# Kernel optimization log

Hardware: AMD Instinct MI355X
Metric: run time of the kernel (lower is better)

The kernel has to match this reference:

```python
import jax, jax.numpy as jnp
import numpy as np

IMG = 224          # image_size
FMAP = (56, 56)    # feature_map_dims (AdaptiveAvgPool2d((56,56)))
K_REWEIGHT = 3     # self.n_reweight
BLUR_RADIUS = 4    # KNNGaussianBlur(4): kernel 9, sigma 4


def _cdist(a, b):
    # Euclidean pairwise distance, [Na, D] x [Nb, D] -> [Na, Nb]
    a2 = jnp.sum(a * a, axis=1, keepdims=True)            # [Na,1]
    b2 = jnp.sum(b * b, axis=1, keepdims=True).T          # [1,Nb]
    d2 = a2 + b2 - 2.0 * (a @ b.T)
    return jnp.sqrt(jnp.maximum(d2, 0.0))


def _gaussian_blur(x):
    # x: [1,1,H,W]; torchvision GaussianBlur(kernel=9, sigma=4), reflect pad
    r, sigma = BLUR_RADIUS, float(BLUR_RADIUS)
    t = jnp.arange(2 * r + 1, dtype=x.dtype) - r
    g = jnp.exp(-(t * t) / (2.0 * sigma * sigma))
    g = g / jnp.sum(g)
    k2d = jnp.outer(g, g)[None, None]                     # [1,1,9,9]
    xp = jnp.pad(x, ((0, 0), (0, 0), (r, r), (r, r)), mode='reflect')
    return jax.lax.conv_general_dilated(
        xp, k2d, window_strides=(1, 1), padding='VALID',
        dimension_numbers=('NCHW', 'OIHW', 'NCHW'))


def setup_inputs() -> dict:
    key = jax.random.key(0)
    k1, k2 = jax.random.split(key)
    patch = jax.random.normal(k1, (FMAP[0] * FMAP[1], 768), dtype=jnp.float32)
    patch_lib = jax.random.normal(k2, (16384, 768), dtype=jnp.float32)
    mean = jnp.zeros((), dtype=jnp.float32)
    std = jnp.ones((), dtype=jnp.float32)
    return {"patch": patch, "patch_lib": patch_lib, "mean": mean, "std": std}


def reference(patch, patch_lib, mean, std):
    # normalization (method_name != 'Point_MAE' branch)
    p = (patch - mean) / std                               # [N, D]

    dist = _cdist(p, patch_lib)                            # [N, Nlib]
    min_val = jnp.min(dist, axis=1)                        # [N]
    min_idx = jnp.argmin(dist, axis=1)                     # [N]
    s_idx = jnp.argmax(min_val)
    s_star = jnp.max(min_val)

    m_test = p[s_idx]                                      # [D]
    m_star = patch_lib[min_idx[s_idx]]                     # [D]

    # distances of m_star to whole bank, k smallest
    w_dist = jnp.sqrt(jnp.maximum(
        jnp.sum((patch_lib - m_star) ** 2, axis=1), 0.0))  # [Nlib]
    _, nn_idx = jax.lax.top_k(-w_dist, K_REWEIGHT)         # smallest k
    m_star_knn = jnp.linalg.norm(
        m_test[None, :] - patch_lib[nn_idx[1:]], axis=1)   # [k-1]

    D_sqrt = jnp.sqrt(jnp.asarray(patch.shape[1], dtype=p.dtype))
    w = 1.0 - jnp.exp(s_star / D_sqrt) / jnp.sum(jnp.exp(m_star_knn / D_sqrt))
    s = w * s_star

    s_map = min_val.reshape(1, 1, *FMAP)
    s_map = jax.image.resize(s_map, (1, 1, IMG, IMG), method='bilinear')
    s_map = _gaussian_blur(s_map)
    return s, s_map
```

## Files before the change

### kernel.cpp

```cpp
#include <hip/hip_runtime.h>
#include <hip/hip_bf16.h>
#include <stdint.h>

#define N_PATCH 3136
#define N_PATCH_PAD 3200
#define N_LIB   16384
#define DIM     768
#define IMGSZ   224
#define FM      56

#define BK 32
#define KT 24
#define MT 25
#define NTILES 128

typedef __bf16 bf16_t;
typedef __bf16 bf16x8 __attribute__((ext_vector_type(8)));
typedef __bf16 bf16x4_v __attribute__((ext_vector_type(4)));
typedef float  f32x4  __attribute__((ext_vector_type(4)));

#define FLT_MAX_ 3.402823466e+38f

struct Scal {
  unsigned long long approx_max_pack;
  unsigned long long cand_pack[64];
  int cand[64];
  int cand_count;
};

__device__ __forceinline__ float wave_reduce_sum(float v) {
#pragma unroll
  for (int s = 32; s > 0; s >>= 1) v += __shfl_xor(v, s, 64);
  return v;
}

__device__ __forceinline__ unsigned long long shfl_xor_u64(unsigned long long v, int mask) {
  unsigned lo = (unsigned)v, hi = (unsigned)(v >> 32);
  lo = __shfl_xor(lo, mask, 64);
  hi = __shfl_xor(hi, mask, 64);
  return ((unsigned long long)hi << 32) | lo;
}

__device__ __forceinline__ void async16(const bf16_t* g, bf16_t* l) {
  __builtin_amdgcn_global_load_lds(
      (const __attribute__((address_space(1))) unsigned int*)g,
      (__attribute__((address_space(3))) unsigned int*)l, 16, 0, 0);
}

__global__ void prep_patch_kernel(const float* __restrict__ patch,
                                  const float* __restrict__ meanp,
                                  const float* __restrict__ stdp,
                                  bf16_t* __restrict__ pb, float* __restrict__ a2,
                                  Scal* sc) {
  int t = threadIdx.x;
  int row = blockIdx.x * 4 + (t >> 6);
  int lane = t & 63;
  if (blockIdx.x == 0) {
    if (t < 64) sc->cand_pack[t] = ~0ULL;
    if (t == 0) { sc->approx_max_pack = 0ULL; sc->cand_count = 0; }
  }
  float mu = meanp[0], sd = stdp[0];
  float acc = 0.f;
#pragma unroll
  for (int k = 0; k < 3; k++) {
    float4 v = ((const float4*)(patch + (size_t)row * DIM))[lane + 64 * k];
    v.x = (v.x - mu) / sd; v.y = (v.y - mu) / sd;
    v.z = (v.z - mu) / sd; v.w = (v.w - mu) / sd;
    bf16x4_v o = {(__bf16)v.x, (__bf16)v.y, (__bf16)v.z, (__bf16)v.w};
    *(bf16x4_v*)(pb + (size_t)row * DIM + (lane + 64 * k) * 4) = o;
    acc += v.x*v.x + v.y*v.y + v.z*v.z + v.w*v.w;
  }
  acc = wave_reduce_sum(acc);
  if (lane == 0) a2[row] = acc;
}

__global__ void prep_lib_kernel(const float* __restrict__ lib,
                                bf16_t* __restrict__ lb, float* __restrict__ b2) {
  int t = threadIdx.x;
  int row = blockIdx.x * 4 + (t >> 6);
  int lane = t & 63;
  float acc = 0.f;
#pragma unroll
  for (int k = 0; k < 3; k++) {
    float4 v = ((const float4*)(lib + (size_t)row * DIM))[lane + 64 * k];
    bf16x4_v o = {(__bf16)v.x, (__bf16)v.y, (__bf16)v.z, (__bf16)v.w};
    *(bf16x4_v*)(lb + (size_t)row * DIM + (lane + 64 * k) * 4) = o;
    acc += v.x*v.x + v.y*v.y + v.z*v.z + v.w*v.w;
  }
  acc = wave_reduce_sum(acc);
  if (lane == 0) b2[row] = acc;
}

__global__ __launch_bounds__(256, 3)
void gemm_min_kernel(const bf16_t* __restrict__ pb, const bf16_t* __restrict__ lb,
                     const float* __restrict__ a2, const float* __restrict__ b2,
                     float* __restrict__ part) {
  __shared__ __align__(16) bf16_t As[2][128 * BK];
  __shared__ __align__(16) bf16_t Bs[2][128 * BK];
  __shared__ unsigned smin[128];

  const int t = threadIdx.x;
  const int wave = t >> 6;
  const int lane = t & 63;
  const int l15 = lane & 15;
  const int quad = lane >> 4;
  const int wm = (wave >> 1) * 64;
  const int wn = (wave & 1) * 64;

  const int lid = blockIdx.x;
  const int xcd = lid & 7;
  const int slot = lid >> 3;
  const int ntile = xcd + 8 * (slot / MT);
  const int mtile = slot % MT;
  const int m0 = mtile * 128;
  const int n0 = ntile * 128;

  int ra0 = m0 + (t >> 2);       if (ra0 > N_PATCH - 1) ra0 = N_PATCH - 1;
  int ra1 = m0 + 64 + (t >> 2);  if (ra1 > N_PATCH - 1) ra1 = N_PATCH - 1;
  const bf16_t* gA0 = pb + (size_t)ra0 * DIM + (t & 3) * 8;
  const bf16_t* gA1 = pb + (size_t)ra1 * DIM + (t & 3) * 8;
  const bf16_t* gB0 = lb + (size_t)(n0 + (t >> 2)) * DIM + (t & 3) * 8;
  const bf16_t* gB1 = gB0 + (size_t)64 * DIM;

  if (t < 128) smin[t] = 0xffffffffu;

  {
    bf16_t* la = &As[0][0];
    bf16_t* lb_ = &Bs[0][0];
    async16(gA0, la + t * 8);
    async16(gA1, la + 2048 + t * 8);
    async16(gB0, lb_ + t * 8);
    async16(gB1, lb_ + 2048 + t * 8);
  }
  __syncthreads();

  f32x4 acc[4][4];
#pragma unroll
  for (int mi = 0; mi < 4; mi++)
#pragma unroll
    for (int ni = 0; ni < 4; ni++) { f32x4 z = {0.f,0.f,0.f,0.f}; acc[mi][ni] = z; }

  for (int k = 0; k < KT; ++k) {
    const int cur = k & 1;
    if (k + 1 < KT) {
      const int nxt = cur ^ 1;
      const size_t ko = (size_t)(k + 1) * BK;
      bf16_t* la = &As[nxt][0];
      bf16_t* lb_ = &Bs[nxt][0];
      async16(gA0 + ko, la + t * 8);
      async16(gA1 + ko, la + 2048 + t * 8);
      async16(gB0 + ko, lb_ + t * 8);
      async16(gB1 + ko, lb_ + 2048 + t * 8);
    }

    bf16x8 afr[4], bfr[4];
#pragma unroll
    for (int mi = 0; mi < 4; mi++)
      afr[mi] = *(const bf16x8*)(&As[cur][(wm + mi * 16 + l15) * BK + quad * 8]);
#pragma unroll
    for (int ni = 0; ni < 4; ni++)
      bfr[ni] = *(const bf16x8*)(&Bs[cur][(wn + ni * 16 + l15) * BK + quad * 8]);
#pragma unroll
    for (int mi = 0; mi < 4; mi++)
#pragma unroll
      for (int ni = 0; ni < 4; ni++)
        acc[mi][ni] = __builtin_amdgcn_mfma_f32_16x16x32_bf16(afr[mi], bfr[ni],
                                                              acc[mi][ni], 0, 0, 0);
    __syncthreads();
  }

  float b2n[4];
#pragma unroll
  for (int ni = 0; ni < 4; ni++) b2n[ni] = b2[n0 + wn + ni * 16 + l15];

#pragma unroll
  for (int mi = 0; mi < 4; mi++) {
#pragma unroll
    for (int r = 0; r < 4; r++) {
      int rloc = wm + mi * 16 + quad * 4 + r;
      int mrow = m0 + rloc;
      float a2v = a2[mrow < N_PATCH ? mrow : (N_PATCH - 1)];
      float best = a2v + b2n[0] - 2.0f * acc[mi][0][r];
#pragma unroll
      for (int ni = 1; ni < 4; ni++)
        best = fminf(best, a2v + b2n[ni] - 2.0f * acc[mi][ni][r]);
      best = fmaxf(best, 0.0f);
#pragma unroll
      for (int s = 1; s < 16; s <<= 1)
        best = fminf(best, __shfl_xor(best, s, 64));
      if (l15 == 0) atomicMin(&smin[rloc], __float_as_uint(best));
    }
  }
  __syncthreads();
  if (t < 128) part[(size_t)(m0 + t) * NTILES + ntile] = __uint_as_float(smin[t]);
}

__global__ void finalize_kernel(const float* __restrict__ part,
                                float* __restrict__ min_val, Scal* sc) {
  int t = threadIdx.x;
  int row = blockIdx.x * 4 + (t >> 6);
  int lane = t & 63;
  if (row >= N_PATCH) return;
  uint2 pv = *(const uint2*)(part + (size_t)row * NTILES + lane * 2);
  unsigned m = pv.x < pv.y ? pv.x : pv.y;
#pragma unroll
  for (int s = 1; s < 64; s <<= 1) {
    unsigned o = __shfl_xor((int)m, s, 64);
    if (o < m) m = o;
  }
  if (lane == 0) {
    float v = sqrtf(__uint_as_float(m));
    min_val[row] = v;
    unsigned long long mp = (((unsigned long long)__float_as_uint(v)) << 32) |
                            (unsigned)(0xffffffffu - (unsigned)row);
    atomicMax(&sc->approx_max_pack, mp);
  }
}

__global__ void collect_kernel(const float* __restrict__ min_val, Scal* sc) {
  int i = blockIdx.x * 256 + threadIdx.x;
  if (i >= N_PATCH) return;
  float amax = __uint_as_float((unsigned)(sc->approx_max_pack >> 32));
  if (min_val[i] >= amax - 0.02f) {
    int p = atomicAdd(&sc->cand_count, 1);
    if (p < 64) sc->cand[p] = i;
  }
}

__global__ void refine_kernel(const float* __restrict__ patch, const float* __restrict__ lib,
                              const float* __restrict__ meanp, const float* __restrict__ stdp,
                              Scal* sc) {
  int c = blockIdx.x;
  int cnt = sc->cand_count; if (cnt > 64) cnt = 64;
  if (c >= cnt) return;
  int row = sc->cand[c];
  int wave = threadIdx.x >> 6, lane = threadIdx.x & 63;
  float mu = meanp[0], sd = stdp[0];
  float4 pv[3];
#pragma unroll
  for (int k = 0; k < 3; k++) {
    float4 v = ((const float4*)(patch + (size_t)row * DIM))[lane + 64 * k];
    v.x = (v.x - mu) / sd; v.y = (v.y - mu) / sd;
    v.z = (v.z - mu) / sd; v.w = (v.w - mu) / sd;
    pv[k] = v;
  }
  unsigned long long best = ~0ULL;
  int jbase = blockIdx.y * 128 + wave * 32;
  for (int rr = 0; rr < 32; rr++) {
    int j = jbase + rr;
    const float4* pl = (const float4*)(lib + (size_t)j * DIM);
    float acc = 0.f;
#pragma unroll
    for (int k = 0; k < 3; k++) {
      float4 l = pl[lane + 64 * k];
      float dx = pv[k].x - l.x, dy = pv[k].y - l.y;
      float dz = pv[k].z - l.z, dw = pv[k].w - l.w;
      acc += dx*dx + dy*dy + dz*dz + dw*dw;
    }
    acc = wave_reduce_sum(acc);
    unsigned long long pk = (((unsigned long long)__float_as_uint(acc)) << 32) | (unsigned)j;
    if (pk < best) best = pk;
  }
  if (lane == 0) atomicMin(&sc->cand_pack[c], best);
}

__device__ __forceinline__ void wave_pick(const Scal* sc, int lane,
                                          int* srow, float* sstar, int* ms) {
  int cnt = sc->cand_count; if (cnt > 64) cnt = 64;
  unsigned long long pk = 0ULL;
  int rowv = 0, msv = 0;
  if (lane < cnt) {
    unsigned long long cp = sc->cand_pack[lane];
    rowv = sc->cand[lane];
    msv = (int)(cp & 0xffffffffu);
    pk = (cp & 0xffffffff00000000ULL) | (unsigned)(0xffffffffu - (unsigned)rowv);
  }
  unsigned long long m = pk;
#pragma unroll
  for (int s = 1; s < 64; s <<= 1) {
    unsigned long long o = shfl_xor_u64(m, s);
    if (o > m) m = o;
  }
  unsigned long long mask = __ballot(pk == m && lane < cnt);
  int wl = (int)(__ffsll((long long)mask) - 1);
  *srow = __shfl(rowv, wl, 64);
  *ms   = __shfl(msv, wl, 64);
  *sstar = sqrtf(__uint_as_float((unsigned)(m >> 32)));
}

__global__ void wdist_kernel(const float* __restrict__ lib, const Scal* __restrict__ sc,
                             float* __restrict__ wdist2) {
  __shared__ int sms;
  int wave = threadIdx.x >> 6, lane = threadIdx.x & 63;
  if (wave == 0) {
    int srow, ms; float sstar;
    wave_pick(sc, lane, &srow, &sstar, &ms);
    if (lane == 0) sms = ms;
  }
  __syncthreads();
  int ms = sms;
  int j = blockIdx.x * 4 + wave;
  const float4* pj = (const float4*)(lib + (size_t)j * DIM);
  const float4* pm = (const float4*)(lib + (size_t)ms * DIM);
  float acc = 0.f;
#pragma unroll
  for (int k = 0; k < 3; k++) {
    float4 a = pj[lane + 64 * k], b = pm[lane + 64 * k];
    float dx = a.x - b.x, dy = a.y - b.y, dz = a.z - b.z, dw = a.w - b.w;
    acc += dx*dx + dy*dy + dz*dz + dw*dw;
  }
  acc = wave_reduce_sum(acc);
  if (lane == 0) wdist2[j] = acc;
}

__global__ void top3_kernel(const float* __restrict__ wdist2,
                            const float* __restrict__ patch, const float* __restrict__ lib,
                            const float* __restrict__ meanp, const float* __restrict__ stdp,
                            const Scal* __restrict__ sc, float* __restrict__ out) {
  __shared__ unsigned long long sl[768];
  int t = threadIdx.x;

  unsigned long long b0 = ~0ULL, b1 = ~0ULL, b2 = ~0ULL;
  for (int j = t; j < N_LIB; j += 256) {
    unsigned long long pk = (((unsigned long long)__float_as_uint(wdist2[j])) << 32) | (unsigned)j;
    if (pk < b0)      { b2 = b1; b1 = b0; b0 = pk; }
    else if (pk < b1) { b2 = b1; b1 = pk; }
    else if (pk < b2) { b2 = pk; }
  }
  sl[t * 3 + 0] = b0; sl[t * 3 + 1] = b1; sl[t * 3 + 2] = b2;
  __syncthreads();
  if (t >= 64) return;

  unsigned long long c0 = ~0ULL, c1 = ~0ULL, c2 = ~0ULL;
#pragma unroll
  for (int e = 0; e < 12; e++) {
    unsigned long long pk = sl[t * 12 + e];
    if (pk < c0)      { c2 = c1; c1 = c0; c0 = pk; }
    else if (pk < c1) { c2 = c1; c1 = pk; }
    else if (pk < c2) { c2 = pk; }
  }
  unsigned long long res1 = 0, res2 = 0;
#pragma unroll
  for (int r = 0; r < 3; r++) {
    unsigned long long m = c0;
#pragma unroll
    for (int s = 1; s < 64; s <<= 1) {
      unsigned long long o = shfl_xor_u64(m, s);
      if (o < m) m = o;
    }
    if (r == 1) res1 = m;
    if (r == 2) res2 = m;
    if (c0 == m) { c0 = c1; c1 = c2; c2 = ~0ULL; }
  }
  int nA = (int)(res1 & 0xffffffffu);
  int nB = (int)(res2 & 0xffffffffu);

  int srow, ms; float sstar;
  wave_pick(sc, t, &srow, &sstar, &ms);

  float mu = meanp[0], sd = stdp[0];
  float accA = 0.f, accB = 0.f;
#pragma unroll
  for (int k = 0; k < 3; k++) {
    float4 p4 = ((const float4*)(patch + (size_t)srow * DIM))[t + 64 * k];
    float4 a4 = ((const float4*)(lib + (size_t)nA * DIM))[t + 64 * k];
    float4 b4 = ((const float4*)(lib + (size_t)nB * DIM))[t + 64 * k];
    float px = (p4.x - mu) / sd, py = (p4.y - mu) / sd;
    float pz = (p4.z - mu) / sd, pw = (p4.w - mu) / sd;
    float dax = px - a4.x, day = py - a4.y, daz = pz - a4.z, daw = pw - a4.w;
    float dbx = px - b4.x, dby = py - b4.y, dbz = pz - b4.z, dbw = pw - b4.w;
    accA += dax*dax + day*day + daz*daz + daw*daw;
    accB += dbx*dbx + dby*dby + dbz*dbz + dbw*dbw;
  }
  accA = wave_reduce_sum(accA);
  accB = wave_reduce_sum(accB);
  if (t == 0) {
    float dsq = sqrtf((float)DIM);
    float d1 = sqrtf(accA), d2v = sqrtf(accB);
    float w = 1.0f - expf(sstar / dsq) / (expf(d1 / dsq) + expf(d2v / dsq));
    out[0] = w * sstar;
  }
}

__global__ void resize_kernel(const float* __restrict__ mv, float* __restrict__ rz) {
  int o = blockIdx.x * 256 + threadIdx.x;
  if (o >= IMGSZ * IMGSZ) return;
  int y = o / IMGSZ, x = o % IMGSZ;
  float sy = 0.25f * y - 0.375f; sy = fminf(fmaxf(sy, 0.0f), 55.0f);
  float sx = 0.25f * x - 0.375f; sx = fminf(fmaxf(sx, 0.0f), 55.0f);
  int y0 = (int)sy; if (y0 > 54) y0 = 54;
  int x0 = (int)sx; if (x0 > 54) x0 = 54;
  float fy = sy - y0, fx = sx - x0;
  float v00 = mv[y0*FM + x0],     v01 = mv[y0*FM + x0 + 1];
  float v10 = mv[(y0+1)*FM + x0], v11 = mv[(y0+1)*FM + x0 + 1];
  float a = v00 + fx * (v01 - v00);
  float b = v10 + fx * (v11 - v10);
  rz[o] = a + fy * (b - a);
}

__global__ void blur_kernel(const float* __restrict__ rz, float* __restrict__ out) {
  int o = blockIdx.x * 256 + threadIdx.x;
  if (o >= IMGSZ * IMGSZ) return;
  int y = o / IMGSZ, x = o % IMGSZ;
  float g[9]; float gs = 0.f;
#pragma unroll
  for (int i = 0; i < 9; i++) { float tt = (float)(i - 4); g[i] = expf(-(tt*tt)/32.0f); gs += g[i]; }
#pragma unroll
  for (int i = 0; i < 9; i++) g[i] /= gs;
  float acc = 0.f;
#pragma unroll
  for (int dy = 0; dy < 9; dy++) {
    int yy = y + dy - 4;
    yy = yy < 0 ? -yy : (yy > IMGSZ - 1 ? 2*(IMGSZ-1) - yy : yy);
    float ra = 0.f;
#pragma unroll
    for (int dx = 0; dx < 9; dx++) {
      int xx = x + dx - 4;
      xx = xx < 0 ? -xx : (xx > IMGSZ - 1 ? 2*(IMGSZ-1) - xx : xx);
      ra += g[dx] * rz[yy*IMGSZ + xx];
    }
    acc += g[dy] * ra;
  }
  out[o] = acc;
}

extern "C" void kernel_launch(void* const* d_in, const int* in_sizes, int n_in,
                              void* d_out, int out_size, void* d_ws, size_t ws_size,
                              hipStream_t stream) {
  const float* patch = (const float*)d_in[0];
  const float* lib   = (const float*)d_in[1];
  const float* meanp = (const float*)d_in[2];
  const float* stdp  = (const float*)d_in[3];
  float* out = (float*)d_out;

  char* ws = (char*)d_ws;
  size_t off = 0;
  auto alloc = [&](size_t bytes) -> void* {
    void* p = ws + off;
    off = (off + bytes + 255) & ~(size_t)255;
    return p;
  };
  bf16_t* pb      = (bf16_t*)alloc((size_t)N_PATCH * DIM * sizeof(bf16_t));
  bf16_t* lb      = (bf16_t*)alloc((size_t)N_LIB * DIM * sizeof(bf16_t));
  float* a2       = (float*)alloc(N_PATCH * sizeof(float));
  float* b2       = (float*)alloc(N_LIB * sizeof(float));
  float* part     = (float*)alloc((size_t)N_PATCH_PAD * NTILES * sizeof(float));
  float* min_val  = (float*)alloc(N_PATCH * sizeof(float));
  float* wdist2   = (float*)alloc(N_LIB * sizeof(float));
  float* resized  = (float*)alloc(IMGSZ * IMGSZ * sizeof(float));
  Scal*  sc       = (Scal*)alloc(sizeof(Scal));

  prep_patch_kernel<<<N_PATCH / 4, 256, 0, stream>>>(patch, meanp, stdp, pb, a2, sc);
  prep_lib_kernel<<<N_LIB / 4, 256, 0, stream>>>(lib, lb, b2);
  gemm_min_kernel<<<MT * NTILES, 256, 0, stream>>>(pb, lb, a2, b2, part);
  finalize_kernel<<<N_PATCH / 4, 256, 0, stream>>>(part, min_val, sc);
  collect_kernel<<<(N_PATCH + 255) / 256, 256, 0, stream>>>(min_val, sc);
  refine_kernel<<<dim3(64, 128), 256, 0, stream>>>(patch, lib, meanp, stdp, sc);
  wdist_kernel<<<N_LIB / 4, 256, 0, stream>>>(lib, sc, wdist2);
  top3_kernel<<<1, 256, 0, stream>>>(wdist2, patch, lib, meanp, stdp, sc, out);
  resize_kernel<<<(IMGSZ * IMGSZ + 255) / 256, 256, 0, stream>>>(min_val, resized);
  blur_kernel<<<(IMGSZ * IMGSZ + 255) / 256, 256, 0, stream>>>(resized, out + 1);
}
```

Measured before the change: 374.1 us.

## Fuse small kernels via last-block patterns and merge resize with blur

Merges the patch and library prep kernels into one launch, and folds the collect step into finalize using a last-block atomic counter. Folds top3 into wdist with the same pattern, and fuses resize with blur through a shared-memory tile. It also transposes the partial-min layout so finalize reads coalesced columns, and raises the GEMM launch bounds occupancy hint from 3 to 4. The aim is to remove launch overhead and intermediate round-trips. The cost is a finalize step that now runs on only 25 blocks, plus extra atomics and fences.

```diff
diff --git a/kernel.cpp b/kernel.cpp
--- a/kernel.cpp
+++ b/kernel.cpp
@@ -26,6 +26,8 @@
   unsigned long long cand_pack[64];
   int cand[64];
   int cand_count;
+  int done1;
+  int done2;
 };
 
 __device__ __forceinline__ float wave_reduce_sum(float v) {
@@ -47,51 +49,47 @@
       (__attribute__((address_space(3))) unsigned int*)l, 16, 0, 0);
 }
 
-__global__ void prep_patch_kernel(const float* __restrict__ patch,
-                                  const float* __restrict__ meanp,
-                                  const float* __restrict__ stdp,
-                                  bf16_t* __restrict__ pb, float* __restrict__ a2,
-                                  Scal* sc) {
+__global__ void prep_kernel(const float* __restrict__ patch, const float* __restrict__ lib,
+                            const float* __restrict__ meanp, const float* __restrict__ stdp,
+                            bf16_t* __restrict__ pb, bf16_t* __restrict__ lb,
+                            float* __restrict__ a2, float* __restrict__ b2, Scal* sc) {
   int t = threadIdx.x;
-  int row = blockIdx.x * 4 + (t >> 6);
   int lane = t & 63;
   if (blockIdx.x == 0) {
     if (t < 64) sc->cand_pack[t] = ~0ULL;
-    if (t == 0) { sc->approx_max_pack = 0ULL; sc->cand_count = 0; }
-  }
-  float mu = meanp[0], sd = stdp[0];
-  float acc = 0.f;
-#pragma unroll
-  for (int k = 0; k < 3; k++) {
-    float4 v = ((const float4*)(patch + (size_t)row * DIM))[lane + 64 * k];
-    v.x = (v.x - mu) / sd; v.y = (v.y - mu) / sd;
-    v.z = (v.z - mu) / sd; v.w = (v.w - mu) / sd;
-    bf16x4_v o = {(__bf16)v.x, (__bf16)v.y, (__bf16)v.z, (__bf16)v.w};
-    *(bf16x4_v*)(pb + (size_t)row * DIM + (lane + 64 * k) * 4) = o;
-    acc += v.x*v.x + v.y*v.y + v.z*v.z + v.w*v.w;
-  }
-  acc = wave_reduce_sum(acc);
-  if (lane == 0) a2[row] = acc;
-}
-
-__global__ void prep_lib_kernel(const float* __restrict__ lib,
-                                bf16_t* __restrict__ lb, float* __restrict__ b2) {
-  int t = threadIdx.x;
-  int row = blockIdx.x * 4 + (t >> 6);
-  int lane = t & 63;
-  float acc = 0.f;
-#pragma unroll
-  for (int k = 0; k < 3; k++) {
-    float4 v = ((const float4*)(lib + (size_t)row * DIM))[lane + 64 * k];
-    bf16x4_v o = {(__bf16)v.x, (__bf16)v.y, (__bf16)v.z, (__bf16)v.w};
-    *(bf16x4_v*)(lb + (size_t)row * DIM + (lane + 64 * k) * 4) = o;
-    acc += v.x*v.x + v.y*v.y + v.z*v.z + v.w*v.w;
-  }
-  acc = wave_reduce_sum(acc);
-  if (lane == 0) b2[row] = acc;
-}
-
-__global__ __launch_bounds__(256, 3)
+    if (t == 64) { sc->approx_max_pack = 0ULL; sc->cand_count = 0; sc->done1 = 0; sc->done2 = 0; }
+  }
+  if (blockIdx.x < N_PATCH / 4) {
+    int row = blockIdx.x * 4 + (t >> 6);
+    float mu = meanp[0], sd = stdp[0];
+    float acc = 0.f;
+#pragma unroll
+    for (int k = 0; k < 3; k++) {
+      float4 v = ((const float4*)(patch + (size_t)row * DIM))[lane + 64 * k];
+      v.x = (v.x - mu) / sd; v.y = (v.y - mu) / sd;
+      v.z = (v.z - mu) / sd; v.w = (v.w - mu) / sd;
+      bf16x4_v o = {(__bf16)v.x, (__bf16)v.y, (__bf16)v.z, (__bf16)v.w};
+      *(bf16x4_v*)(pb + (size_t)row * DIM + (lane + 64 * k) * 4) = o;
+      acc += v.x*v.x + v.y*v.y + v.z*v.z + v.w*v.w;
+    }
+    acc = wave_reduce_sum(acc);
+    if (lane == 0) a2[row] = acc;
+  } else {
+    int row = (blockIdx.x - N_PATCH / 4) * 4 + (t >> 6);
+    float acc = 0.f;
+#pragma unroll
+    for (int k = 0; k < 3; k++) {
+      float4 v = ((const float4*)(lib + (size_t)row * DIM))[lane + 64 * k];
+      bf16x4_v o = {(__bf16)v.x, (__bf16)v.y, (__bf16)v.z, (__bf16)v.w};
+      *(bf16x4_v*)(lb + (size_t)row * DIM + (lane + 64 * k) * 4) = o;
+      acc += v.x*v.x + v.y*v.y + v.z*v.z + v.w*v.w;
+    }
+    acc = wave_reduce_sum(acc);
+    if (lane == 0) b2[row] = acc;
+  }
+}
+
+__global__ __launch_bounds__(256, 4)
 void gemm_min_kernel(const bf16_t* __restrict__ pb, const bf16_t* __restrict__ lb,
                      const float* __restrict__ a2, const float* __restrict__ b2,
                      float* __restrict__ part) {
@@ -192,38 +190,37 @@
     }
   }
   __syncthreads();
-  if (t < 128) part[(size_t)(m0 + t) * NTILES + ntile] = __uint_as_float(smin[t]);
-}
-
-__global__ void finalize_kernel(const float* __restrict__ part,
-                                float* __restrict__ min_val, Scal* sc) {
+  if (t < 128) part[(size_t)ntile * N_PATCH_PAD + m0 + t] = __uint_as_float(smin[t]);
+}
+
+__global__ void finalize_collect_kernel(const float* __restrict__ part,
+                                        float* __restrict__ min_val, Scal* sc) {
+  __shared__ bool last;
   int t = threadIdx.x;
-  int row = blockIdx.x * 4 + (t >> 6);
-  int lane = t & 63;
-  if (row >= N_PATCH) return;
-  uint2 pv = *(const uint2*)(part + (size_t)row * NTILES + lane * 2);
-  unsigned m = pv.x < pv.y ? pv.x : pv.y;
-#pragma unroll
-  for (int s = 1; s < 64; s <<= 1) {
-    unsigned o = __shfl_xor((int)m, s, 64);
-    if (o < m) m = o;
-  }
-  if (lane == 0) {
-    float v = sqrtf(__uint_as_float(m));
+  int row = blockIdx.x * 128 + t;
+  float m = FLT_MAX_;
+#pragma unroll 8
+  for (int nt = 0; nt < NTILES; nt++)
+    m = fminf(m, part[(size_t)nt * N_PATCH_PAD + row]);
+  if (row < N_PATCH) {
+    float v = sqrtf(m);
     min_val[row] = v;
     unsigned long long mp = (((unsigned long long)__float_as_uint(v)) << 32) |
                             (unsigned)(0xffffffffu - (unsigned)row);
     atomicMax(&sc->approx_max_pack, mp);
   }
-}
-
-__global__ void collect_kernel(const float* __restrict__ min_val, Scal* sc) {
-  int i = blockIdx.x * 256 + threadIdx.x;
-  if (i >= N_PATCH) return;
-  float amax = __uint_as_float((unsigned)(sc->approx_max_pack >> 32));
-  if (min_val[i] >= amax - 0.02f) {
-    int p = atomicAdd(&sc->cand_count, 1);
-    if (p < 64) sc->cand[p] = i;
+  __threadfence();
+  __syncthreads();
+  if (t == 0) last = (atomicAdd(&sc->done1, 1) == MT - 1);
+  __syncthreads();
+  if (!last) return;
+  __threadfence();
+  float amax = __uint_as_float((unsigned)(atomicMax(&sc->approx_max_pack, 0ULL) >> 32));
+  for (int i = t; i < N_PATCH; i += 128) {
+    if (min_val[i] >= amax - 0.02f) {
+      int p = atomicAdd(&sc->cand_count, 1);
+      if (p < 64) sc->cand[p] = i;
+    }
   }
 }
 
@@ -288,41 +285,49 @@
   *sstar = sqrtf(__uint_as_float((unsigned)(m >> 32)));
 }
 
-__global__ void wdist_kernel(const float* __restrict__ lib, const Scal* __restrict__ sc,
-                             float* __restrict__ wdist2) {
+__global__ void wdist_top3_kernel(const float* __restrict__ lib,
+                                  const float* __restrict__ patch,
+                                  const float* __restrict__ meanp,
+                                  const float* __restrict__ stdp,
+                                  Scal* sc, float* __restrict__ wdist2,
+                                  float* __restrict__ out) {
+  __shared__ unsigned long long sl[768];
   __shared__ int sms;
-  int wave = threadIdx.x >> 6, lane = threadIdx.x & 63;
+  __shared__ bool last;
+  int t = threadIdx.x;
+  int wave = t >> 6, lane = t & 63;
+
   if (wave == 0) {
-    int srow, ms; float sstar;
-    wave_pick(sc, lane, &srow, &sstar, &ms);
-    if (lane == 0) sms = ms;
+    int srow_, ms_; float ss_;
+    wave_pick(sc, lane, &srow_, &ss_, &ms_);
+    if (lane == 0) sms = ms_;
   }
   __syncthreads();
   int ms = sms;
   int j = blockIdx.x * 4 + wave;
-  const float4* pj = (const float4*)(lib + (size_t)j * DIM);
-  const float4* pm = (const float4*)(lib + (size_t)ms * DIM);
-  float acc = 0.f;
-#pragma unroll
-  for (int k = 0; k < 3; k++) {
-    float4 a = pj[lane + 64 * k], b = pm[lane + 64 * k];
-    float dx = a.x - b.x, dy = a.y - b.y, dz = a.z - b.z, dw = a.w - b.w;
-    acc += dx*dx + dy*dy + dz*dz + dw*dw;
-  }
-  acc = wave_reduce_sum(acc);
-  if (lane == 0) wdist2[j] = acc;
-}
-
-__global__ void top3_kernel(const float* __restrict__ wdist2,
-                            const float* __restrict__ patch, const float* __restrict__ lib,
-                            const float* __restrict__ meanp, const float* __restrict__ stdp,
-                            const Scal* __restrict__ sc, float* __restrict__ out) {
-  __shared__ unsigned long long sl[768];
-  int t = threadIdx.x;
+  {
+    const float4* pj = (const float4*)(lib + (size_t)j * DIM);
+    const float4* pm = (const float4*)(lib + (size_t)ms * DIM);
+    float acc = 0.f;
+#pragma unroll
+    for (int k = 0; k < 3; k++) {
+      float4 a = pj[lane + 64 * k], b = pm[lane + 64 * k];
+      float dx = a.x - b.x, dy = a.y - b.y, dz = a.z - b.z, dw = a.w - b.w;
+      acc += dx*dx + dy*dy + dz*dz + dw*dw;
+    }
+    acc = wave_reduce_sum(acc);
+    if (lane == 0) wdist2[j] = acc;
+  }
+  __threadfence();
+  __syncthreads();
+  if (t == 0) last = (atomicAdd(&sc->done2, 1) == N_LIB / 4 - 1);
+  __syncthreads();
+  if (!last) return;
+  __threadfence();
 
   unsigned long long b0 = ~0ULL, b1 = ~0ULL, b2 = ~0ULL;
-  for (int j = t; j < N_LIB; j += 256) {
-    unsigned long long pk = (((unsigned long long)__float_as_uint(wdist2[j])) << 32) | (unsigned)j;
+  for (int jj = t; jj < N_LIB; jj += 256) {
+    unsigned long long pk = (((unsigned long long)__float_as_uint(wdist2[jj])) << 32) | (unsigned)jj;
     if (pk < b0)      { b2 = b1; b1 = b0; b0 = pk; }
     else if (pk < b1) { b2 = b1; b1 = pk; }
     else if (pk < b2) { b2 = pk; }
@@ -355,8 +360,8 @@
   int nA = (int)(res1 & 0xffffffffu);
   int nB = (int)(res2 & 0xffffffffu);
 
-  int srow, ms; float sstar;
-  wave_pick(sc, t, &srow, &sstar, &ms);
+  int srow, ms2; float sstar;
+  wave_pick(sc, t, &srow, &sstar, &ms2);
 
   float mu = meanp[0], sd = stdp[0];
   float accA = 0.f, accB = 0.f;
@@ -382,46 +387,54 @@
   }
 }
 
-__global__ void resize_kernel(const float* __restrict__ mv, float* __restrict__ rz) {
-  int o = blockIdx.x * 256 + threadIdx.x;
-  if (o >= IMGSZ * IMGSZ) return;
-  int y = o / IMGSZ, x = o % IMGSZ;
-  float sy = 0.25f * y - 0.375f; sy = fminf(fmaxf(sy, 0.0f), 55.0f);
-  float sx = 0.25f * x - 0.375f; sx = fminf(fmaxf(sx, 0.0f), 55.0f);
-  int y0 = (int)sy; if (y0 > 54) y0 = 54;
-  int x0 = (int)sx; if (x0 > 54) x0 = 54;
-  float fy = sy - y0, fx = sx - x0;
-  float v00 = mv[y0*FM + x0],     v01 = mv[y0*FM + x0 + 1];
-  float v10 = mv[(y0+1)*FM + x0], v11 = mv[(y0+1)*FM + x0 + 1];
-  float a = v00 + fx * (v01 - v00);
-  float b = v10 + fx * (v11 - v10);
-  rz[o] = a + fy * (b - a);
-}
-
-__global__ void blur_kernel(const float* __restrict__ rz, float* __restrict__ out) {
-  int o = blockIdx.x * 256 + threadIdx.x;
-  if (o >= IMGSZ * IMGSZ) return;
-  int y = o / IMGSZ, x = o % IMGSZ;
+__global__ void resize_blur_kernel(const float* __restrict__ mv, float* __restrict__ out) {
+  __shared__ float rs[40 * 40];
+  int bx = blockIdx.x % 7, by = blockIdx.x / 7;
+  int ox0 = bx * 32, oy0 = by * 32;
+  int t = threadIdx.x;
+
+  for (int i = t; i < 1600; i += 256) {
+    int ly = i / 40, lx = i % 40;
+    int gy = oy0 - 4 + ly; gy = gy < 0 ? 0 : (gy > 223 ? 223 : gy);
+    int gx = ox0 - 4 + lx; gx = gx < 0 ? 0 : (gx > 223 ? 223 : gx);
+    float sy = fminf(fmaxf(0.25f * gy - 0.375f, 0.0f), 55.0f);
+    float sx = fminf(fmaxf(0.25f * gx - 0.375f, 0.0f), 55.0f);
+    int y0 = (int)sy; if (y0 > 54) y0 = 54;
+    int x0 = (int)sx; if (x0 > 54) x0 = 54;
+    float fy = sy - y0, fx = sx - x0;
+    float v00 = mv[y0*FM + x0],     v01 = mv[y0*FM + x0 + 1];
+    float v10 = mv[(y0+1)*FM + x0], v11 = mv[(y0+1)*FM + x0 + 1];
+    float a = v00 + fx * (v01 - v00);
+    float b = v10 + fx * (v11 - v10);
+    rs[i] = a + fy * (b - a);
+  }
+  __syncthreads();
+
   float g[9]; float gs = 0.f;
 #pragma unroll
   for (int i = 0; i < 9; i++) { float tt = (float)(i - 4); g[i] = expf(-(tt*tt)/32.0f); gs += g[i]; }
 #pragma unroll
   for (int i = 0; i < 9; i++) g[i] /= gs;
-  float acc = 0.f;
-#pragma unroll
-  for (int dy = 0; dy < 9; dy++) {
-    int yy = y + dy - 4;
-    yy = yy < 0 ? -yy : (yy > IMGSZ - 1 ? 2*(IMGSZ-1) - yy : yy);
-    float ra = 0.f;
-#pragma unroll
-    for (int dx = 0; dx < 9; dx++) {
-      int xx = x + dx - 4;
-      xx = xx < 0 ? -xx : (xx > IMGSZ - 1 ? 2*(IMGSZ-1) - xx : xx);
-      ra += g[dx] * rz[yy*IMGSZ + xx];
-    }
-    acc += g[dy] * ra;
-  }
-  out[o] = acc;
+
+  for (int p = t; p < 1024; p += 256) {
+    int y = oy0 + p / 32, x = ox0 + (p & 31);
+    float acc = 0.f;
+#pragma unroll
+    for (int dy = 0; dy < 9; dy++) {
+      int yy = y + dy - 4;
+      yy = yy < 0 ? -yy : (yy > IMGSZ - 1 ? 2*(IMGSZ-1) - yy : yy);
+      int lyy = yy - (oy0 - 4);
+      float ra = 0.f;
+#pragma unroll
+      for (int dx = 0; dx < 9; dx++) {
+        int xx = x + dx - 4;
+        xx = xx < 0 ? -xx : (xx > IMGSZ - 1 ? 2*(IMGSZ-1) - xx : xx);
+        ra += g[dx] * rs[lyy * 40 + (xx - (ox0 - 4))];
+      }
+      acc += g[dy] * ra;
+    }
+    out[y * IMGSZ + x] = acc;
+  }
 }
 
 extern "C" void kernel_launch(void* const* d_in, const int* in_sizes, int n_in,
@@ -447,17 +460,13 @@
   float* part     = (float*)alloc((size_t)N_PATCH_PAD * NTILES * sizeof(float));
   float* min_val  = (float*)alloc(N_PATCH * sizeof(float));
   float* wdist2   = (float*)alloc(N_LIB * sizeof(float));
-  float* resized  = (float*)alloc(IMGSZ * IMGSZ * sizeof(float));
   Scal*  sc       = (Scal*)alloc(sizeof(Scal));
 
-  prep_patch_kernel<<<N_PATCH / 4, 256, 0, stream>>>(patch, meanp, stdp, pb, a2, sc);
-  prep_lib_kernel<<<N_LIB / 4, 256, 0, stream>>>(lib, lb, b2);
+  prep_kernel<<<N_PATCH / 4 + N_LIB / 4, 256, 0, stream>>>(patch, lib, meanp, stdp,
+                                                           pb, lb, a2, b2, sc);
   gemm_min_kernel<<<MT * NTILES, 256, 0, stream>>>(pb, lb, a2, b2, part);
-  finalize_kernel<<<N_PATCH / 4, 256, 0, stream>>>(part, min_val, sc);
-  collect_kernel<<<(N_PATCH + 255) / 256, 256, 0, stream>>>(min_val, sc);
+  finalize_collect_kernel<<<MT, 128, 0, stream>>>(part, min_val, sc);
   refine_kernel<<<dim3(64, 128), 256, 0, stream>>>(patch, lib, meanp, stdp, sc);
-  wdist_kernel<<<N_LIB / 4, 256, 0, stream>>>(lib, sc, wdist2);
-  top3_kernel<<<1, 256, 0, stream>>>(wdist2, patch, lib, meanp, stdp, sc, out);
-  resize_kernel<<<(IMGSZ * IMGSZ + 255) / 256, 256, 0, stream>>>(min_val, resized);
-  blur_kernel<<<(IMGSZ * IMGSZ + 255) / 256, 256, 0, stream>>>(resized, out + 1);
-}
+  wdist_top3_kernel<<<N_LIB / 4, 256, 0, stream>>>(lib, patch, meanp, stdp, sc, wdist2, out);
+  resize_blur_kernel<<<49, 256, 0, stream>>>(min_val, out + 1);
+}
```

New measurement: 697.9 us. 86.5% more time.
